# Performance work log

Hardware: AMD Instinct MI355X
Metric: run time of the kernel (lower is better)

Reference implementation:

```python
import jax, jax.numpy as jnp
import numpy as np

B, C, D, E, ES, TOPK = 8, 4096, 1024, 16, 256, 4096

def setup_inputs() -> dict:
    key = jax.random.key(0)
    k1, k2, k3, k4 = jax.random.split(key, 4)
    x = jax.random.normal(k1, (B, C, D), dtype=jnp.float32)
    gate = jax.random.normal(k2, (C, E), dtype=jnp.float32) / np.sqrt(D)
    lin1_weight = jax.random.normal(k3, (D, E, ES), dtype=jnp.float32) / np.sqrt(D)
    lin2_weight = jax.random.normal(k4, (E, ES, D), dtype=jnp.float32) / np.sqrt(ES)
    return {"x": x, "gate": gate, "lin1_weight": lin1_weight, "lin2_weight": lin2_weight, "topk": TOPK}

def reference(x, gate, lin1_weight, lin2_weight, topk):
    b, c, d = x.shape
    e = gate.shape[1]
    n_tokens = b * c
    # faithful to original einsum: sum x over dmodel, elementwise-mult by gate[c, e]
    gate_out = jnp.einsum('bcd,ce->bce', x, gate)            # [b, c, e]
    gate_out = jnp.transpose(gate_out, (2, 0, 1)).reshape(e, n_tokens)
    gate_out = jax.nn.softmax(gate_out, axis=1)              # softmax over tokens per expert
    topk_values, topk_indices = jax.lax.top_k(gate_out, topk)  # [e, k]
    xf = x.reshape(n_tokens, d)
    flat_idx = topk_indices.reshape(-1)
    gathered = xf[flat_idx].reshape(e, topk, d)              # dispatch
    h = jax.nn.relu(jnp.einsum('ekd,des->eks', gathered, lin1_weight))
    out = jnp.einsum('eks,esd->ekd', h, lin2_weight)
    out = out * topk_values[..., None]                       # weight by gate probs
    z = jnp.zeros_like(xf).at[flat_idx].add(out.reshape(-1, d))  # scatter-add combine
    return z.reshape(b, c, d)
```

## Files before the change

### kernel.cpp

```cpp
#include <hip/hip_runtime.h>
#include <hip/hip_bf16.h>

#define BB 8
#define CC 4096
#define DD 1024
#define EE 16
#define ESS 256
#define KSEL 4096
#define NTOK (BB*CC)

typedef short bf16x8 __attribute__((ext_vector_type(8)));
typedef float f32x4 __attribute__((ext_vector_type(4)));
typedef unsigned u32x4 __attribute__((ext_vector_type(4)));

struct PickRes { unsigned tau; unsigned n_gt; unsigned n_tie; float sm; };

__device__ __forceinline__ short f2bf(float f) {
  unsigned u = __float_as_uint(f);
  u += 0x7FFFu + ((u >> 16) & 1u);
  return (short)(u >> 16);
}
__device__ __forceinline__ float bf2f(short s) {
  return __uint_as_float(((unsigned)(unsigned short)s) << 16);
}
__device__ __forceinline__ unsigned f2key(float f) {
  unsigned u = __float_as_uint(f);
  return (u & 0x80000000u) ? ~u : (u | 0x80000000u);
}

#define ASG __attribute__((address_space(1)))
#define ASL __attribute__((address_space(3)))
__device__ __forceinline__ void gl_lds16(void* l, const void* g) {
  __builtin_amdgcn_global_load_lds((ASG const unsigned*)g, (ASL unsigned*)l, 16, 0, 0);
}

__global__ void k_logits(const float* __restrict__ x, const float* __restrict__ gate,
                         float* __restrict__ logits, short* __restrict__ xb,
                         int* __restrict__ inv) {
  int wid = threadIdx.x >> 6, lane = threadIdx.x & 63;
  int t = blockIdx.x * 4 + wid;
  const float4* xr = reinterpret_cast<const float4*>(x + (size_t)t * DD);
  short4* xw = reinterpret_cast<short4*>(xb + (size_t)t * DD);
  float s = 0.f;
#pragma unroll
  for (int i = 0; i < 4; ++i) {
    float4 v = xr[lane + 64 * i];
    s += v.x + v.y + v.z + v.w;
    short4 p;
    p.x = f2bf(v.x); p.y = f2bf(v.y); p.z = f2bf(v.z); p.w = f2bf(v.w);
    xw[lane + 64 * i] = p;
  }
#pragma unroll
  for (int off = 32; off; off >>= 1) s += __shfl_xor(s, off);
  if (lane < EE) {
    int c = t & (CC - 1);
    logits[(size_t)lane * NTOK + t] = s * gate[c * EE + lane];
    inv[(size_t)t * EE + lane] = -1;
  }
}

__global__ __launch_bounds__(1024) void k_hist(const float* __restrict__ logits,
                                               unsigned* __restrict__ ghist,
                                               float* __restrict__ separt) {
  int e = blockIdx.x & 15, seg = blockIdx.x >> 4;
  const float* L = logits + (size_t)e * NTOK + seg * 4096;
  unsigned* Hh = ghist + (size_t)e * 65536;
  int tid = threadIdx.x;
  float sl = 0.f;
#pragma unroll
  for (int i = 0; i < 4; ++i) {
    float lv = L[tid + 1024 * i];
    atomicAdd(&Hh[f2key(lv) >> 16], 1u);
    sl += expf(lv);
  }
  __shared__ float red[1024];
  red[tid] = sl; __syncthreads();
  for (int s2 = 512; s2; s2 >>= 1) {
    if (tid < s2) red[tid] += red[tid + s2];
    __syncthreads();
  }
  if (tid == 0) separt[e * 8 + seg] = red[0];
}

__global__ __launch_bounds__(1024) void k_pick(const unsigned* __restrict__ ghist,
                                               const float* __restrict__ logits,
                                               const float* __restrict__ separt,
                                               PickRes* __restrict__ pres,
                                               unsigned* __restrict__ bases) {
  int e = blockIdx.x;
  const unsigned* Hh = ghist + (size_t)e * 65536;
  const float* L = logits + (size_t)e * NTOK;
  int tid = threadIdx.x;
  __shared__ unsigned u0[1024], u1[1024];
  __shared__ unsigned hist256[256];
  __shared__ unsigned sh_b16, sh_ngt, sh_kth;
  __shared__ unsigned sh_p24, sh_ngt2, sh_kth2;
  __shared__ unsigned sh_tau;
  __shared__ unsigned sgc[8], sqc[8];

  unsigned cs = 0;
  for (int j = 0; j < 64; ++j) cs += Hh[tid * 64 + j];
  u0[tid] = cs; __syncthreads();
  unsigned* src = u0; unsigned* dst = u1;
  for (int d2 = 1; d2 < 1024; d2 <<= 1) {
    unsigned v = src[tid] + ((tid + d2 < 1024) ? src[tid + d2] : 0u);
    dst[tid] = v; __syncthreads();
    unsigned* tmp = src; src = dst; dst = tmp;
  }
  unsigned kth0 = KSEL;
  unsigned above = (tid < 1023) ? src[tid + 1] : 0u;
  if (above < kth0 && kth0 <= src[tid]) {
    unsigned cum = above;
    for (int j = 63; j >= 0; --j) {
      unsigned h = Hh[tid * 64 + j];
      if (cum + h >= kth0) { sh_b16 = (unsigned)(tid * 64 + j); sh_ngt = cum; sh_kth = kth0 - cum; break; }
      cum += h;
    }
  }
  __syncthreads();
  unsigned p16 = sh_b16, ngt1 = sh_ngt, kth1 = sh_kth;

  if (tid < 256) hist256[tid] = 0;
  __syncthreads();
  for (int t = tid; t < NTOK; t += 1024) {
    unsigned key = f2key(L[t]);
    if ((key >> 16) == p16) atomicAdd(&hist256[(key >> 8) & 255], 1u);
  }
  __syncthreads();
  if (tid == 0) {
    unsigned cum = 0; int d = 255;
    for (; d >= 0; --d) { unsigned h = hist256[d]; if (cum + h >= kth1) break; cum += h; }
    sh_p24 = (p16 << 8) | (unsigned)d;
    sh_ngt2 = ngt1 + cum;
    sh_kth2 = kth1 - cum;
  }
  __syncthreads();
  unsigned p24 = sh_p24, ngt2 = sh_ngt2, kth2 = sh_kth2;

  if (tid < 256) hist256[tid] = 0;
  __syncthreads();
  for (int t = tid; t < NTOK; t += 1024) {
    unsigned key = f2key(L[t]);
    if ((key >> 8) == p24) atomicAdd(&hist256[key & 255], 1u);
  }
  __syncthreads();
  if (tid == 0) {
    unsigned cum = 0; int d = 255;
    for (; d >= 0; --d) { unsigned h = hist256[d]; if (cum + h >= kth2) break; cum += h; }
    unsigned tau = (p24 << 8) | (unsigned)d;
    unsigned n_gt = ngt2 + cum;
    float sm = 0.f;
    for (int j = 0; j < 8; ++j) sm += separt[e * 8 + j];
    PickRes pr; pr.tau = tau; pr.n_gt = n_gt; pr.n_tie = KSEL - n_gt; pr.sm = sm;
    pres[e] = pr;
    sh_tau = tau;
  }
  if (tid < 8) { sgc[tid] = 0; sqc[tid] = 0; }
  __syncthreads();
  unsigned tau = sh_tau;
  for (int t = tid; t < NTOK; t += 1024) {
    unsigned key = f2key(L[t]);
    unsigned long long bg = __ballot(key > tau);
    unsigned long long bq = __ballot(key == tau);
    if ((tid & 63) == 0) {
      int seg = t >> 12;
      if (bg) atomicAdd(&sgc[seg], (unsigned)__popcll(bg));
      if (bq) atomicAdd(&sqc[seg], (unsigned)__popcll(bq));
    }
  }
  __syncthreads();
  if (tid == 0) {
    unsigned gb = 0, qb = 0;
    for (int s = 0; s < 8; ++s) {
      bases[e * 8 + s] = (gb << 16) | qb;
      gb += sgc[s]; qb += sqc[s];
    }
  }
}

__global__ __launch_bounds__(1024) void k_compact(const float* __restrict__ logits,
                                                  const PickRes* __restrict__ pres,
                                                  const unsigned* __restrict__ bases,
                                                  int* __restrict__ sel_idx,
                                                  float* __restrict__ sel_val,
                                                  int* __restrict__ inv) {
  int e = blockIdx.x & 15, seg = blockIdx.x >> 4;
  PickRes pr = pres[e];
  const float* L = logits + (size_t)e * NTOK;
  unsigned b = bases[e * 8 + seg];
  __shared__ unsigned wtg[16], wtq[16];
  __shared__ unsigned base_g, base_q;
  int tid = threadIdx.x, wid = tid >> 6, lane = tid & 63;
  if (tid == 0) { base_g = b >> 16; base_q = b & 0xFFFFu; }
  __syncthreads();
#pragma unroll 1
  for (int i = 0; i < 4; ++i) {
    int t = seg * 4096 + tid + 1024 * i;
    float lv = L[t];
    unsigned key = f2key(lv);
    bool g = key > pr.tau, q = key == pr.tau;
    unsigned long long bg = __ballot(g), bq = __ballot(q);
    unsigned long long lm = (1ull << lane) - 1ull;
    unsigned pg = __popcll(bg & lm), pq = __popcll(bq & lm);
    if (lane == 63) { wtg[wid] = pg + (g ? 1u : 0u); wtq[wid] = pq + (q ? 1u : 0u); }
    __syncthreads();
    unsigned og = base_g, oq = base_q;
    for (int w2 = 0; w2 < wid; ++w2) { og += wtg[w2]; oq += wtq[w2]; }
    unsigned slot = 0xFFFFFFFFu;
    if (g) slot = og + pg;
    else if (q) {
      unsigned r = oq + pq;
      if (r < pr.n_tie) slot = pr.n_gt + r;
    }
    if (slot != 0xFFFFFFFFu) {
      sel_idx[(size_t)e * KSEL + slot] = t;
      sel_val[(size_t)e * KSEL + slot] = expf(lv) / pr.sm;
      inv[(size_t)t * EE + e] = e * KSEL + (int)slot;
    }
    __syncthreads();
    if (tid == 0) {
      unsigned sg = 0, sq = 0;
#pragma unroll
      for (int w2 = 0; w2 < 16; ++w2) { sg += wtg[w2]; sq += wtq[w2]; }
      base_g += sg; base_q += sq;
    }
    __syncthreads();
  }
}

__global__ void k_transpose(const float* __restrict__ src, short* __restrict__ dst,
                            int R, int C) {
  __shared__ float tile[64][65];
  int c0 = blockIdx.x * 64, r0 = blockIdx.y * 64, b = blockIdx.z;
  const float* S = src + (size_t)b * R * C;
  short* Dp = dst + (size_t)b * R * C;
  int tx = threadIdx.x & 63, ty = threadIdx.x >> 6;
#pragma unroll
  for (int i = 0; i < 16; ++i) {
    int r = ty + 4 * i;
    tile[r][tx] = S[(size_t)(r0 + r) * C + c0 + tx];
  }
  __syncthreads();
#pragma unroll
  for (int i = 0; i < 16; ++i) {
    int cR = ty + 4 * i;
    Dp[(size_t)(c0 + cR) * R + r0 + tx] = f2bf(tile[tx][cR]);
  }
}

__global__ __launch_bounds__(512, 4) void k_ff(
    const short* __restrict__ xb, const short* __restrict__ W1T,
    const short* __restrict__ W2T, const int* __restrict__ sel_idx,
    const float* __restrict__ sel_val, short* __restrict__ out) {
  int bid = blockIdx.x;
  int e = (bid & 7) + ((bid >> 9) << 3);
  int m0 = ((bid >> 3) & 63) * 64;
  __shared__ short Hl[64 * 256];
  __shared__ bf16x8 As8[64 * 8];
  __shared__ bf16x8 Bs8[256 * 8];
  int tid = threadIdx.x, lane = tid & 63, wid = tid >> 6;
  int wr = wid >> 2, wc = wid & 3;
  const int* idxE = sel_idx + (size_t)e * KSEL;
  f32x4 acc[2][4] = {};

  int rowA = tid >> 3, sA = tid & 7;
  int xk = rowA & 7;
  const short* aSrc = xb + (size_t)idxE[m0 + rowA] * DD + (sA ^ xk) * 8;
  const short* w1Base = W1T + (size_t)e * ESS * DD + (size_t)rowA * DD + (sA ^ xk) * 8;
  const short* w2Base = W2T + (size_t)e * DD * ESS + (size_t)rowA * ESS + (sA ^ xk) * 8;

  for (int kt = 0; kt < DD / 64; ++kt) {
    int kofs = kt * 64;
    gl_lds16(&As8[tid], aSrc + kofs);
#pragma unroll
    for (int j = 0; j < 4; ++j)
      gl_lds16(&Bs8[j * 512 + tid], w1Base + (size_t)(64 * j) * DD + kofs);
    __syncthreads();
    bf16x8 af[2][2];
#pragma unroll
    for (int mg = 0; mg < 2; ++mg) {
      int row = wr * 32 + mg * 16 + (lane & 15);
#pragma unroll
      for (int h = 0; h < 2; ++h) {
        int seg = h * 4 + (lane >> 4);
        af[mg][h] = As8[row * 8 + (seg ^ (row & 7))];
      }
    }
#pragma unroll
    for (int ng = 0; ng < 4; ++ng) {
      int rowb = wc * 64 + ng * 16 + (lane & 15);
      bf16x8 b0 = Bs8[rowb * 8 + (((lane >> 4) + 0) ^ (rowb & 7))];
      bf16x8 b1 = Bs8[rowb * 8 + (((lane >> 4) + 4) ^ (rowb & 7))];
#pragma unroll
      for (int mg = 0; mg < 2; ++mg) {
        acc[mg][ng] = __builtin_amdgcn_mfma_f32_16x16x32_bf16(af[mg][0], b0, acc[mg][ng], 0, 0, 0);
        acc[mg][ng] = __builtin_amdgcn_mfma_f32_16x16x32_bf16(af[mg][1], b1, acc[mg][ng], 0, 0, 0);
      }
    }
    __syncthreads();
  }
#pragma unroll
  for (int mg = 0; mg < 2; ++mg) {
#pragma unroll
    for (int r = 0; r < 4; ++r) {
      int hrow = wr * 32 + mg * 16 + (lane >> 4) * 4 + r;
      float v = sel_val[(size_t)e * KSEL + m0 + hrow];
#pragma unroll
      for (int ng = 0; ng < 4; ++ng) {
        int col = wc * 64 + ng * 16 + (lane & 15);
        int sic = (col >> 3) & 7;
        int idx = hrow * 256 + ((col >> 6) * 8 + (sic ^ (hrow & 7))) * 8 + (col & 7);
        Hl[idx] = f2bf(fmaxf(acc[mg][ng][r], 0.f) * v);
      }
    }
  }
  __syncthreads();
#pragma unroll 1
  for (int np = 0; np < 4; ++np) {
    int n0 = np * 256;
    f32x4 acc2[2][4] = {};
#pragma unroll 1
    for (int kt = 0; kt < ESS / 64; ++kt) {
      int kofs = kt * 64;
#pragma unroll
      for (int j = 0; j < 4; ++j)
        gl_lds16(&Bs8[j * 512 + tid], w2Base + (size_t)(n0 + 64 * j) * ESS + kofs);
      __syncthreads();
      bf16x8 af[2][2];
#pragma unroll
      for (int mg = 0; mg < 2; ++mg) {
        int row = wr * 32 + mg * 16 + (lane & 15);
#pragma unroll
        for (int h = 0; h < 2; ++h) {
          int s8 = h * 4 + (lane >> 4);
          af[mg][h] = *reinterpret_cast<const bf16x8*>(
              &Hl[row * 256 + (kt * 8 + (s8 ^ (row & 7))) * 8]);
        }
      }
#pragma unroll
      for (int ng = 0; ng < 4; ++ng) {
        int rowb = wc * 64 + ng * 16 + (lane & 15);
        bf16x8 b0 = Bs8[rowb * 8 + (((lane >> 4) + 0) ^ (rowb & 7))];
        bf16x8 b1 = Bs8[rowb * 8 + (((lane >> 4) + 4) ^ (rowb & 7))];
#pragma unroll
        for (int mg = 0; mg < 2; ++mg) {
          acc2[mg][ng] = __builtin_amdgcn_mfma_f32_16x16x32_bf16(af[mg][0], b0, acc2[mg][ng], 0, 0, 0);
          acc2[mg][ng] = __builtin_amdgcn_mfma_f32_16x16x32_bf16(af[mg][1], b1, acc2[mg][ng], 0, 0, 0);
        }
      }
      __syncthreads();
    }
#pragma unroll
    for (int mg = 0; mg < 2; ++mg) {
#pragma unroll
      for (int r = 0; r < 4; ++r) {
        int ml = wr * 32 + mg * 16 + (lane >> 4) * 4 + r;
        short* orow = out + ((size_t)(e * KSEL + m0 + ml)) * DD + n0 + wc * 64 + (lane & 15);
#pragma unroll
        for (int ng = 0; ng < 4; ++ng) orow[ng * 16] = f2bf(acc2[mg][ng][r]);
      }
    }
  }
}

__global__ __launch_bounds__(512, 4) void k_gemm1(
    const short* __restrict__ xb, const short* __restrict__ W1T,
    const int* __restrict__ sel_idx, const float* __restrict__ sel_val,
    short* __restrict__ H) {
  int bid = blockIdx.x;
  int m0 = ((bid >> 3) & 31) * 128;
  int e = (bid & 7) + ((bid >> 8) << 3);
  __shared__ bf16x8 As8[128 * 8];
  __shared__ bf16x8 Bs8[256 * 8];
  int tid = threadIdx.x, lane = tid & 63, wid = tid >> 6;
  int wr = wid >> 2, wc = wid & 3;
  const int* idxE = sel_idx + (size_t)e * KSEL;
  f32x4 acc[4][4] = {};

  int rowA = tid >> 3, sA = tid & 7;
  int xk = rowA & 7;
  const short* aSrc0 = xb + (size_t)idxE[m0 + rowA] * DD + (sA ^ xk) * 8;
  const short* aSrc1 = xb + (size_t)idxE[m0 + rowA + 64] * DD + (sA ^ xk) * 8;
  const short* wBase = W1T + (size_t)e * ESS * DD + (size_t)rowA * DD + (sA ^ xk) * 8;

  for (int kt = 0; kt < DD / 64; ++kt) {
    int kofs = kt * 64;
    gl_lds16(&As8[tid], aSrc0 + kofs);
    gl_lds16(&As8[512 + tid], aSrc1 + kofs);
#pragma unroll
    for (int j = 0; j < 4; ++j)
      gl_lds16(&Bs8[j * 512 + tid], wBase + (size_t)(64 * j) * DD + kofs);
    __syncthreads();
    bf16x8 af[4][2];
#pragma unroll
    for (int mg = 0; mg < 4; ++mg) {
      int row = wr * 64 + mg * 16 + (lane & 15);
#pragma unroll
      for (int h = 0; h < 2; ++h) {
        int seg = h * 4 + (lane >> 4);
        af[mg][h] = As8[row * 8 + (seg ^ (row & 7))];
      }
    }
#pragma unroll
    for (int ng = 0; ng < 4; ++ng) {
      int rowb = wc * 64 + ng * 16 + (lane & 15);
      bf16x8 b0 = Bs8[rowb * 8 + (((lane >> 4) + 0) ^ (rowb & 7))];
      bf16x8 b1 = Bs8[rowb * 8 + (((lane >> 4) + 4) ^ (rowb & 7))];
#pragma unroll
      for (int mg = 0; mg < 4; ++mg) {
        acc[mg][ng] = __builtin_amdgcn_mfma_f32_16x16x32_bf16(af[mg][0], b0, acc[mg][ng], 0, 0, 0);
        acc[mg][ng] = __builtin_amdgcn_mfma_f32_16x16x32_bf16(af[mg][1], b1, acc[mg][ng], 0, 0, 0);
      }
    }
    __syncthreads();
  }
#pragma unroll
  for (int mg = 0; mg < 4; ++mg) {
#pragma unroll
    for (int r = 0; r < 4; ++r) {
      int ml = wr * 64 + mg * 16 + (lane >> 4) * 4 + r;
      float v = sel_val[(size_t)e * KSEL + m0 + ml];
      short* hrow = H + ((size_t)(e * KSEL + m0 + ml)) * ESS + wc * 64 + (lane & 15);
#pragma unroll
      for (int ng = 0; ng < 4; ++ng) {
        float o = fmaxf(acc[mg][ng][r], 0.f) * v;
        hrow[ng * 16] = f2bf(o);
      }
    }
  }
}

__global__ __launch_bounds__(512, 4) void k_gemm2_atomic(
    const short* __restrict__ H, const short* __restrict__ W2T,
    const int* __restrict__ sel_idx, float* __restrict__ z) {
  int bid = blockIdx.x;
  int p = (bid & 7) + ((bid >> 8) << 3);
  int m0 = ((bid >> 3) & 31) * 128;
  int n0 = (p & 3) * 256;
  int e = p >> 2;
  __shared__ bf16x8 As8[128 * 8];
  __shared__ bf16x8 Bs8[256 * 8];
  int tid = threadIdx.x, lane = tid & 63, wid = tid >> 6;
  int wr = wid >> 2, wc = wid & 3;
  f32x4 acc[4][4] = {};

  int rowA = tid >> 3, sA = tid & 7;
  int xk = rowA & 7;
  const short* hBase = H + (size_t)(e * KSEL + m0 + rowA) * ESS + (sA ^ xk) * 8;
  const short* w2Base = W2T + (size_t)(e * DD + n0 + rowA) * ESS + (sA ^ xk) * 8;

  for (int kt = 0; kt < ESS / 64; ++kt) {
    int kofs = kt * 64;
    gl_lds16(&As8[tid], hBase + kofs);
    gl_lds16(&As8[512 + tid], hBase + (size_t)64 * ESS + kofs);
#pragma unroll
    for (int j = 0; j < 4; ++j)
      gl_lds16(&Bs8[j * 512 + tid], w2Base + (size_t)(64 * j) * ESS + kofs);
    __syncthreads();
    bf16x8 af[4][2];
#pragma unroll
    for (int mg = 0; mg < 4; ++mg) {
      int row = wr * 64 + mg * 16 + (lane & 15);
#pragma unroll
      for (int h = 0; h < 2; ++h) {
        int seg = h * 4 + (lane >> 4);
        af[mg][h] = As8[row * 8 + (seg ^ (row & 7))];
      }
    }
#pragma unroll
    for (int ng = 0; ng < 4; ++ng) {
      int rowb = wc * 64 + ng * 16 + (lane & 15);
      bf16x8 b0 = Bs8[rowb * 8 + (((lane >> 4) + 0) ^ (rowb & 7))];
      bf16x8 b1 = Bs8[rowb * 8 + (((lane >> 4) + 4) ^ (rowb & 7))];
#pragma unroll
      for (int mg = 0; mg < 4; ++mg) {
        acc[mg][ng] = __builtin_amdgcn_mfma_f32_16x16x32_bf16(af[mg][0], b0, acc[mg][ng], 0, 0, 0);
        acc[mg][ng] = __builtin_amdgcn_mfma_f32_16x16x32_bf16(af[mg][1], b1, acc[mg][ng], 0, 0, 0);
      }
    }
    __syncthreads();
  }
#pragma unroll
  for (int mg = 0; mg < 4; ++mg) {
#pragma unroll
    for (int r = 0; r < 4; ++r) {
      int ml = wr * 64 + mg * 16 + (lane >> 4) * 4 + r;
      int token = sel_idx[(size_t)e * KSEL + m0 + ml];
      float* zr = z + (size_t)token * DD + n0 + wc * 64 + (lane & 15);
#pragma unroll
      for (int ng = 0; ng < 4; ++ng) atomicAdd(zr + ng * 16, acc[mg][ng][r]);
    }
  }
}

__global__ __launch_bounds__(256) void k_combine(const short* __restrict__ out,
                                                 const int* __restrict__ inv,
                                                 float* __restrict__ z) {
  int wid = threadIdx.x >> 6, lane = threadIdx.x & 63;
  int tA = (blockIdx.x * 4 + wid) * 2;
  int tB = tA + 1;
  int gA[16], gB[16];
  const int4* ivA = reinterpret_cast<const int4*>(inv + (size_t)tA * EE);
  const int4* ivB = reinterpret_cast<const int4*>(inv + (size_t)tB * EE);
#pragma unroll
  for (int q = 0; q < 4; ++q) {
    int4 va = ivA[q];
    gA[4 * q] = va.x; gA[4 * q + 1] = va.y; gA[4 * q + 2] = va.z; gA[4 * q + 3] = va.w;
    int4 vb = ivB[q];
    gB[4 * q] = vb.x; gB[4 * q + 1] = vb.y; gB[4 * q + 2] = vb.z; gB[4 * q + 3] = vb.w;
  }
  float accA[16] = {}, accB[16] = {};
#pragma unroll
  for (int e = 0; e < EE; ++e) {
    if (gA[e] >= 0) {
      const u32x4* rp = reinterpret_cast<const u32x4*>(out + (size_t)gA[e] * DD + lane * 16);
      u32x4 v0 = rp[0], v1 = rp[1];
      const short* s0 = reinterpret_cast<const short*>(&v0);
      const short* s1 = reinterpret_cast<const short*>(&v1);
#pragma unroll
      for (int i = 0; i < 8; ++i) accA[i] += bf2f(s0[i]);
#pragma unroll
      for (int i = 0; i < 8; ++i) accA[8 + i] += bf2f(s1[i]);
    }
    if (gB[e] >= 0) {
      const u32x4* rp = reinterpret_cast<const u32x4*>(out + (size_t)gB[e] * DD + lane * 16);
      u32x4 v0 = rp[0], v1 = rp[1];
      const short* s0 = reinterpret_cast<const short*>(&v0);
      const short* s1 = reinterpret_cast<const short*>(&v1);
#pragma unroll
      for (int i = 0; i < 8; ++i) accB[i] += bf2f(s0[i]);
#pragma unroll
      for (int i = 0; i < 8; ++i) accB[8 + i] += bf2f(s1[i]);
    }
  }
  float4* zwA = reinterpret_cast<float4*>(z + (size_t)tA * DD + lane * 16);
  float4* zwB = reinterpret_cast<float4*>(z + (size_t)tB * DD + lane * 16);
#pragma unroll
  for (int i = 0; i < 4; ++i) {
    float4 oa;
    oa.x = accA[4 * i]; oa.y = accA[4 * i + 1]; oa.z = accA[4 * i + 2]; oa.w = accA[4 * i + 3];
    zwA[i] = oa;
    float4 ob;
    ob.x = accB[4 * i]; ob.y = accB[4 * i + 1]; ob.z = accB[4 * i + 2]; ob.w = accB[4 * i + 3];
    zwB[i] = ob;
  }
}

extern "C" void kernel_launch(void* const* d_in, const int* in_sizes, int n_in,
                              void* d_out, int out_size, void* d_ws, size_t ws_size,
                              hipStream_t stream) {
  (void)in_sizes; (void)n_in;
  const float* x = (const float*)d_in[0];
  const float* gate = (const float*)d_in[1];
  const float* lin1 = (const float*)d_in[2];
  const float* lin2 = (const float*)d_in[3];
  float* z = (float*)d_out;

  char* ws = (char*)d_ws;
  size_t off = 0;
  auto alloc = [&](size_t bytes) -> void* {
    off = (off + 255) & ~(size_t)255;
    void* p = ws + off;
    off += bytes;
    return p;
  };
  float* logits = (float*)alloc((size_t)EE * NTOK * 4);
  int* sidx = (int*)alloc((size_t)EE * KSEL * 4);
  float* sval = (float*)alloc((size_t)EE * KSEL * 4);
  int* inv = (int*)alloc((size_t)NTOK * EE * 4);
  short* W1T = (short*)alloc((size_t)EE * ESS * DD * 2);
  short* W2T = (short*)alloc((size_t)EE * DD * ESS * 2);
  short* H = (short*)alloc((size_t)EE * KSEL * ESS * 2);
  short* xb = (short*)alloc((size_t)NTOK * DD * 2);
  size_t out_bytes = (size_t)EE * KSEL * DD * 2;
  bool combine = (off + 256 + out_bytes) <= ws_size;
  short* outbuf = combine ? (short*)alloc(out_bytes) : nullptr;

  unsigned* ghist = (unsigned*)H;
  float* separt = (float*)((char*)H + (size_t)EE * 65536 * 4);
  PickRes* pres = (PickRes*)((char*)separt + 1024);
  unsigned* bases = (unsigned*)((char*)pres + 1024);

  k_transpose<<<dim3(64, 16, 1), 256, 0, stream>>>(lin1, W1T, DD, EE * ESS);
  k_transpose<<<dim3(16, 4, 16), 256, 0, stream>>>(lin2, W2T, ESS, DD);
  k_logits<<<NTOK / 4, 256, 0, stream>>>(x, gate, logits, xb, inv);
  hipMemsetAsync(ghist, 0, (size_t)EE * 65536 * 4, stream);
  k_hist<<<128, 1024, 0, stream>>>(logits, ghist, separt);
  k_pick<<<EE, 1024, 0, stream>>>(ghist, logits, separt, pres, bases);
  k_compact<<<128, 1024, 0, stream>>>(logits, pres, bases, sidx, sval, inv);
  if (combine) {
    k_ff<<<1024, 512, 0, stream>>>(xb, W1T, W2T, sidx, sval, outbuf);
    k_combine<<<NTOK / 8, 256, 0, stream>>>(outbuf, inv, z);
  } else {
    hipMemsetAsync(d_out, 0, (size_t)out_size * sizeof(float), stream);
    k_gemm1<<<512, 512, 0, stream>>>(xb, W1T, sidx, sval, H);
    k_gemm2_atomic<<<2048, 512, 0, stream>>>(H, W2T, sidx, z);
  }
}
```

Measured before the change: 326.0 us.

## Split top-k threshold pick into parallel multi-block refine, count and scan kernels

The single-block-per-expert k_pick, which streamed all 32K logits three times with only 16 blocks, is replaced by a two-level 16-bit radix select. Each level is a 64K-bin scan kernel, with a 128-block refine histogram in between, followed by a 128-block count kernel and a tiny scan for segment bases. This spreads the threshold selection across more CUs at the cost of extra kernel launches. Separately, the k_ff hidden tile swaps its XOR swizzle for a padded row stride (264) to avoid LDS bank conflicts with simpler addressing.

```diff
diff --git a/kernel.cpp b/kernel.cpp
--- a/kernel.cpp
+++ b/kernel.cpp
@@ -8,12 +8,14 @@
 #define ESS 256
 #define KSEL 4096
 #define NTOK (BB*CC)
+#define HLS 264
 
 typedef short bf16x8 __attribute__((ext_vector_type(8)));
 typedef float f32x4 __attribute__((ext_vector_type(4)));
 typedef unsigned u32x4 __attribute__((ext_vector_type(4)));
 
 struct PickRes { unsigned tau; unsigned n_gt; unsigned n_tie; float sm; };
+struct Sel1 { unsigned b; unsigned above; unsigned kth; };
 
 __device__ __forceinline__ short f2bf(float f) {
   unsigned u = __float_as_uint(f);
@@ -82,22 +84,16 @@
   if (tid == 0) separt[e * 8 + seg] = red[0];
 }
 
-__global__ __launch_bounds__(1024) void k_pick(const unsigned* __restrict__ ghist,
-                                               const float* __restrict__ logits,
-                                               const float* __restrict__ separt,
-                                               PickRes* __restrict__ pres,
-                                               unsigned* __restrict__ bases) {
+__global__ __launch_bounds__(1024) void k_scan64k(
+    const unsigned* __restrict__ hist, const Sel1* __restrict__ s1in, int phase,
+    Sel1* __restrict__ s1out, const float* __restrict__ separt,
+    PickRes* __restrict__ pres) {
   int e = blockIdx.x;
-  const unsigned* Hh = ghist + (size_t)e * 65536;
-  const float* L = logits + (size_t)e * NTOK;
+  const unsigned* Hh = hist + (size_t)e * 65536;
   int tid = threadIdx.x;
   __shared__ unsigned u0[1024], u1[1024];
-  __shared__ unsigned hist256[256];
-  __shared__ unsigned sh_b16, sh_ngt, sh_kth;
-  __shared__ unsigned sh_p24, sh_ngt2, sh_kth2;
-  __shared__ unsigned sh_tau;
-  __shared__ unsigned sgc[8], sqc[8];
-
+  __shared__ unsigned sh_b, sh_above, sh_kth;
+  unsigned target = (phase == 1) ? (unsigned)KSEL : s1in[e].kth;
   unsigned cs = 0;
   for (int j = 0; j < 64; ++j) cs += Hh[tid * 64 + j];
   u0[tid] = cs; __syncthreads();
@@ -107,73 +103,76 @@
     dst[tid] = v; __syncthreads();
     unsigned* tmp = src; src = dst; dst = tmp;
   }
-  unsigned kth0 = KSEL;
   unsigned above = (tid < 1023) ? src[tid + 1] : 0u;
-  if (above < kth0 && kth0 <= src[tid]) {
+  if (above < target && target <= src[tid]) {
     unsigned cum = above;
     for (int j = 63; j >= 0; --j) {
       unsigned h = Hh[tid * 64 + j];
-      if (cum + h >= kth0) { sh_b16 = (unsigned)(tid * 64 + j); sh_ngt = cum; sh_kth = kth0 - cum; break; }
+      if (cum + h >= target) { sh_b = (unsigned)(tid * 64 + j); sh_above = cum; sh_kth = target - cum; break; }
       cum += h;
     }
-  }
-  __syncthreads();
-  unsigned p16 = sh_b16, ngt1 = sh_ngt, kth1 = sh_kth;
-
-  if (tid < 256) hist256[tid] = 0;
-  __syncthreads();
-  for (int t = tid; t < NTOK; t += 1024) {
-    unsigned key = f2key(L[t]);
-    if ((key >> 16) == p16) atomicAdd(&hist256[(key >> 8) & 255], 1u);
   }
   __syncthreads();
   if (tid == 0) {
-    unsigned cum = 0; int d = 255;
-    for (; d >= 0; --d) { unsigned h = hist256[d]; if (cum + h >= kth1) break; cum += h; }
-    sh_p24 = (p16 << 8) | (unsigned)d;
-    sh_ngt2 = ngt1 + cum;
-    sh_kth2 = kth1 - cum;
-  }
-  __syncthreads();
-  unsigned p24 = sh_p24, ngt2 = sh_ngt2, kth2 = sh_kth2;
-
-  if (tid < 256) hist256[tid] = 0;
-  __syncthreads();
-  for (int t = tid; t < NTOK; t += 1024) {
-    unsigned key = f2key(L[t]);
-    if ((key >> 8) == p24) atomicAdd(&hist256[key & 255], 1u);
-  }
-  __syncthreads();
-  if (tid == 0) {
-    unsigned cum = 0; int d = 255;
-    for (; d >= 0; --d) { unsigned h = hist256[d]; if (cum + h >= kth2) break; cum += h; }
-    unsigned tau = (p24 << 8) | (unsigned)d;
-    unsigned n_gt = ngt2 + cum;
-    float sm = 0.f;
-    for (int j = 0; j < 8; ++j) sm += separt[e * 8 + j];
-    PickRes pr; pr.tau = tau; pr.n_gt = n_gt; pr.n_tie = KSEL - n_gt; pr.sm = sm;
-    pres[e] = pr;
-    sh_tau = tau;
-  }
-  if (tid < 8) { sgc[tid] = 0; sqc[tid] = 0; }
-  __syncthreads();
-  unsigned tau = sh_tau;
-  for (int t = tid; t < NTOK; t += 1024) {
-    unsigned key = f2key(L[t]);
-    unsigned long long bg = __ballot(key > tau);
-    unsigned long long bq = __ballot(key == tau);
-    if ((tid & 63) == 0) {
-      int seg = t >> 12;
-      if (bg) atomicAdd(&sgc[seg], (unsigned)__popcll(bg));
-      if (bq) atomicAdd(&sqc[seg], (unsigned)__popcll(bq));
-    }
-  }
-  __syncthreads();
-  if (tid == 0) {
+    if (phase == 1) {
+      Sel1 s; s.b = sh_b; s.above = sh_above; s.kth = sh_kth;
+      s1out[e] = s;
+    } else {
+      unsigned tau = (s1in[e].b << 16) | sh_b;
+      unsigned n_gt = s1in[e].above + sh_above;
+      float sm = 0.f;
+      for (int j = 0; j < 8; ++j) sm += separt[e * 8 + j];
+      PickRes pr; pr.tau = tau; pr.n_gt = n_gt; pr.n_tie = KSEL - n_gt; pr.sm = sm;
+      pres[e] = pr;
+    }
+  }
+}
+
+__global__ __launch_bounds__(1024) void k_refine(const float* __restrict__ logits,
+                                                 const Sel1* __restrict__ s1,
+                                                 unsigned* __restrict__ hist2) {
+  int e = blockIdx.x & 15, seg = blockIdx.x >> 4;
+  unsigned p16 = s1[e].b;
+  const float* L = logits + (size_t)e * NTOK + seg * 4096;
+  unsigned* Hh = hist2 + (size_t)e * 65536;
+  int tid = threadIdx.x;
+#pragma unroll
+  for (int i = 0; i < 4; ++i) {
+    unsigned key = f2key(L[tid + 1024 * i]);
+    if ((key >> 16) == p16) atomicAdd(&Hh[key & 0xFFFF], 1u);
+  }
+}
+
+__global__ __launch_bounds__(1024) void k_count(const float* __restrict__ logits,
+                                                const PickRes* __restrict__ pres,
+                                                unsigned* __restrict__ cnts) {
+  int e = blockIdx.x & 15, seg = blockIdx.x >> 4;
+  PickRes pr = pres[e];
+  const float* L = logits + (size_t)e * NTOK + seg * 4096;
+  int tid = threadIdx.x;
+  unsigned pk = 0;
+#pragma unroll
+  for (int i = 0; i < 4; ++i) {
+    unsigned key = f2key(L[tid + 1024 * i]);
+    pk += (key > pr.tau) ? 0x10000u : ((key == pr.tau) ? 1u : 0u);
+  }
+  __shared__ unsigned red[1024];
+  red[tid] = pk; __syncthreads();
+  for (int s2 = 512; s2; s2 >>= 1) {
+    if (tid < s2) red[tid] += red[tid + s2];
+    __syncthreads();
+  }
+  if (tid == 0) cnts[e * 8 + seg] = red[0];
+}
+
+__global__ void k_scan(const unsigned* __restrict__ cnts, unsigned* __restrict__ bases) {
+  int e = threadIdx.x;
+  if (e < EE) {
     unsigned gb = 0, qb = 0;
     for (int s = 0; s < 8; ++s) {
+      unsigned c = cnts[e * 8 + s];
       bases[e * 8 + s] = (gb << 16) | qb;
-      gb += sgc[s]; qb += sqc[s];
+      gb += c >> 16; qb += c & 0xFFFFu;
     }
   }
 }
@@ -255,7 +254,7 @@
   int bid = blockIdx.x;
   int e = (bid & 7) + ((bid >> 9) << 3);
   int m0 = ((bid >> 3) & 63) * 64;
-  __shared__ short Hl[64 * 256];
+  __shared__ short Hl[64 * HLS];
   __shared__ bf16x8 As8[64 * 8];
   __shared__ bf16x8 Bs8[256 * 8];
   int tid = threadIdx.x, lane = tid & 63, wid = tid >> 6;
@@ -308,9 +307,7 @@
 #pragma unroll
       for (int ng = 0; ng < 4; ++ng) {
         int col = wc * 64 + ng * 16 + (lane & 15);
-        int sic = (col >> 3) & 7;
-        int idx = hrow * 256 + ((col >> 6) * 8 + (sic ^ (hrow & 7))) * 8 + (col & 7);
-        Hl[idx] = f2bf(fmaxf(acc[mg][ng][r], 0.f) * v);
+        Hl[hrow * HLS + col] = f2bf(fmaxf(acc[mg][ng][r], 0.f) * v);
       }
     }
   }
@@ -333,8 +330,7 @@
 #pragma unroll
         for (int h = 0; h < 2; ++h) {
           int s8 = h * 4 + (lane >> 4);
-          af[mg][h] = *reinterpret_cast<const bf16x8*>(
-              &Hl[row * 256 + (kt * 8 + (s8 ^ (row & 7))) * 8]);
+          af[mg][h] = *reinterpret_cast<const bf16x8*>(&Hl[row * HLS + kt * 64 + s8 * 8]);
         }
       }
 #pragma unroll
@@ -577,16 +573,23 @@
   short* outbuf = combine ? (short*)alloc(out_bytes) : nullptr;
 
   unsigned* ghist = (unsigned*)H;
-  float* separt = (float*)((char*)H + (size_t)EE * 65536 * 4);
-  PickRes* pres = (PickRes*)((char*)separt + 1024);
-  unsigned* bases = (unsigned*)((char*)pres + 1024);
+  unsigned* hist2 = (unsigned*)((char*)H + (size_t)4 * 1024 * 1024);
+  float* separt = (float*)((char*)H + (size_t)8 * 1024 * 1024);
+  Sel1* s1 = (Sel1*)((char*)separt + 1024);
+  PickRes* pres = (PickRes*)((char*)s1 + 1024);
+  unsigned* cnts = (unsigned*)((char*)pres + 1024);
+  unsigned* bases = (unsigned*)((char*)cnts + 1024);
 
   k_transpose<<<dim3(64, 16, 1), 256, 0, stream>>>(lin1, W1T, DD, EE * ESS);
   k_transpose<<<dim3(16, 4, 16), 256, 0, stream>>>(lin2, W2T, ESS, DD);
   k_logits<<<NTOK / 4, 256, 0, stream>>>(x, gate, logits, xb, inv);
-  hipMemsetAsync(ghist, 0, (size_t)EE * 65536 * 4, stream);
+  hipMemsetAsync(ghist, 0, (size_t)8 * 1024 * 1024, stream);
   k_hist<<<128, 1024, 0, stream>>>(logits, ghist, separt);
-  k_pick<<<EE, 1024, 0, stream>>>(ghist, logits, separt, pres, bases);
+  k_scan64k<<<EE, 1024, 0, stream>>>(ghist, s1, 1, s1, separt, pres);
+  k_refine<<<128, 1024, 0, stream>>>(logits, s1, hist2);
+  k_scan64k<<<EE, 1024, 0, stream>>>(hist2, s1, 2, s1, separt, pres);
+  k_count<<<128, 1024, 0, stream>>>(logits, pres, cnts);
+  k_scan<<<1, 64, 0, stream>>>(cnts, bases);
   k_compact<<<128, 1024, 0, stream>>>(logits, pres, bases, sidx, sval, inv);
   if (combine) {
     k_ff<<<1024, 512, 0, stream>>>(xb, W1T, W2T, sidx, sval, outbuf);
```

Measured after the change: 313.9 us. -3.7%, faster.
